# Kernel optimization log

Hardware: AMD Instinct MI355X
Metric: run time of the kernel (lower is better)

Reference implementation:

```python
import jax, jax.numpy as jnp
import numpy as np
from jax import lax

H = 100          # hidden_size
IN = 100         # input_size
NUM_LAYERS = 2   # options.LSTMLayer
B = 128
T = 1024


def _uniform(key, shape, bound):
    return jax.random.uniform(key, shape, jnp.float32, -bound, bound)


def setup_inputs() -> dict:
    key = jax.random.key(0)
    ks = jax.random.split(key, 16)
    bound = 1.0 / np.sqrt(H)  # torch nn.LSTM default init
    x = jax.random.normal(ks[0], (B, IN, T), jnp.float32)
    # layer 0: input dim IN; layer 1: input dim 2*H. Stacked over 2 directions.
    w_ih0 = _uniform(ks[1], (2, 4 * H, IN), bound)
    w_hh0 = _uniform(ks[2], (2, 4 * H, H), bound)
    b0 = _uniform(ks[3], (2, 4 * H), bound) + _uniform(ks[4], (2, 4 * H), bound)  # b_ih + b_hh
    w_ih1 = _uniform(ks[5], (2, 4 * H, 2 * H), bound)
    w_hh1 = _uniform(ks[6], (2, 4 * H, H), bound)
    b1 = _uniform(ks[7], (2, 4 * H), bound) + _uniform(ks[8], (2, 4 * H), bound)
    return {"x": x, "w_ih0": w_ih0, "w_hh0": w_hh0, "b0": b0,
            "w_ih1": w_ih1, "w_hh1": w_hh1, "b1": b1}


def _lstm_dir(x, w_ih, w_hh, b):
    # x: (T,B,D). Precompute input-to-gate GEMM once, then scan the recurrence.
    gx = jnp.einsum('tbd,gd->tbg', x, w_ih) + b  # (T,B,4H)
    h0 = jnp.zeros((x.shape[1], H), x.dtype)
    c0 = jnp.zeros((x.shape[1], H), x.dtype)

    def step(carry, g):
        h, c = carry
        gates = g + h @ w_hh.T
        i, f, gg, o = jnp.split(gates, 4, axis=-1)  # torch gate order i,f,g,o
        i = jax.nn.sigmoid(i)
        f = jax.nn.sigmoid(f)
        gg = jnp.tanh(gg)
        o = jax.nn.sigmoid(o)
        c = f * c + i * gg
        h = o * jnp.tanh(c)
        return (h, c), h

    _, hs = lax.scan(step, (h0, c0), gx)
    return hs  # (T,B,H)


def _bilstm_layer(x, w_ih, w_hh, b):
    fwd = _lstm_dir(x, w_ih[0], w_hh[0], b[0])
    bwd = _lstm_dir(x[::-1], w_ih[1], w_hh[1], b[1])[::-1]
    return jnp.concatenate([fwd, bwd], axis=-1)  # (T,B,2H)


def reference(x, w_ih0, w_hh0, b0, w_ih1, w_hh1, b1):
    # x: (B, 100, T) -> permute([2,0,1]) -> (T, B, 100)
    h = jnp.transpose(x, (2, 0, 1))
    h = _bilstm_layer(h, w_ih0, w_hh0, b0)
    h = _bilstm_layer(h, w_ih1, w_hh1, b1)
    return h  # (T, B, 2H), matching nn.LSTM `output`
```

## Files before the change

kernel.cpp:

```cpp
#include <hip/hip_runtime.h>
#include <hip/hip_bf16.h>
#include <stdint.h>

typedef unsigned short ushort_t;
typedef __attribute__((ext_vector_type(8))) short short8;
typedef __attribute__((ext_vector_type(4))) short short4_t;
typedef __attribute__((ext_vector_type(4))) float f32x4;

#define TT 1024
#define BB 128
#define NG 400
#define HID 100

#define ALIGN256(x) ((((size_t)(x)) + 255) & ~(size_t)255)

static const size_t WS_FLAG = 0;
static const size_t WS_XT   = 4096;
static const size_t WS_OUT0 = WS_XT   + (size_t)1024 * 128 * 128 * 2;
static const size_t WS_GX   = WS_OUT0 + (size_t)1024 * 128 * 256 * 2;
static const size_t WS_WIH0 = WS_GX   + (size_t)2 * 1024 * 128 * 400 * 2;
static const size_t WS_WHH  = WS_WIH0 + (size_t)2 * 400 * 128 * 2;
static const size_t WS_WIH1 = WS_WHH  + (size_t)2 * 2 * 400 * 128 * 2;
static const size_t WS_BIAS = WS_WIH1 + (size_t)2 * 400 * 256 * 2;

__device__ __forceinline__ float bf2f(ushort_t v) {
  return __builtin_bit_cast(float, ((unsigned)v) << 16);
}
__device__ __forceinline__ ushort_t f2bf(float f) {
  unsigned u = __builtin_bit_cast(unsigned, f);
  u += 0x7FFF + ((u >> 16) & 1);
  return (ushort_t)(u >> 16);
}
__device__ __forceinline__ ushort_t ldbf(const void* p, size_t i, int isbf) {
  return isbf ? ((const ushort_t*)p)[i] : f2bf(((const float*)p)[i]);
}
__device__ __forceinline__ float ldf(const void* p, size_t i, int isbf) {
  return isbf ? bf2f(((const ushort_t*)p)[i]) : ((const float*)p)[i];
}
__device__ __forceinline__ float fexp2(float x) {
#if __has_builtin(__builtin_amdgcn_exp2f)
  return __builtin_amdgcn_exp2f(x);
#else
  return __exp2f(x);
#endif
}
__device__ __forceinline__ float frcp(float x) {
#if __has_builtin(__builtin_amdgcn_rcpf)
  return __builtin_amdgcn_rcpf(x);
#else
  return 1.0f / x;
#endif
}
__device__ __forceinline__ float sigm(float x) {
  return frcp(1.0f + fexp2(-1.44269504f * x));
}
__device__ __forceinline__ float tanh_(float x) {
  return 1.0f - 2.0f * frcp(1.0f + fexp2(2.88539008f * x));
}

__global__ __launch_bounds__(256) void detect_dtype(const ushort_t* __restrict__ x,
                                                    int* __restrict__ flag) {
  __shared__ int cnt;
  if (threadIdx.x == 0) cnt = 0;
  __syncthreads();
  int local = 0;
  for (int i = threadIdx.x; i < 4096; i += 256) {
    ushort_t u = x[2 * i];
    int e = (u >> 7) & 0xFF;
    if (e >= 0x66 && e <= 0x85) local++;
  }
  atomicAdd(&cnt, local);
  __syncthreads();
  if (threadIdx.x == 0) *flag = (cnt >= 2048) ? 1 : 0;
}

__global__ __launch_bounds__(256) void prep_weights(
    const void* __restrict__ wih0, const void* __restrict__ whh0,
    const void* __restrict__ b0,   const void* __restrict__ wih1,
    const void* __restrict__ whh1, const void* __restrict__ b1,
    ushort_t* __restrict__ WIH0, ushort_t* __restrict__ WHH,
    ushort_t* __restrict__ WIH1, float* __restrict__ BIAS,
    const int* __restrict__ flag)
{
  const int isbf = *flag;
  int tid = blockIdx.x * blockDim.x + threadIdx.x;
  int nth = gridDim.x * blockDim.x;
  for (int idx = tid; idx < 2 * NG * 128; idx += nth) {
    int k = idx & 127; int np = (idx >> 7) % NG; int d = idx / (NG * 128);
    int n = (np & 3) * HID + (np >> 2);
    WIH0[idx] = (k < HID) ? ldbf(wih0, (size_t)(d * NG + n) * 100 + k, isbf) : (ushort_t)0;
  }
  for (int idx = tid; idx < 2 * 2 * NG * 128; idx += nth) {
    int k = idx & 127; int np = (idx >> 7) % NG; int dl = idx / (NG * 128);
    int d = dl & 1; int l = dl >> 1;
    int n = (np & 3) * HID + (np >> 2);
    const void* src = l ? whh1 : whh0;
    WHH[idx] = (k < HID) ? ldbf(src, (size_t)(d * NG + n) * 100 + k, isbf) : (ushort_t)0;
  }
  for (int idx = tid; idx < 2 * NG * 256; idx += nth) {
    int k = idx & 255; int np = (idx >> 8) % NG; int d = idx / (NG * 256);
    int n = (np & 3) * HID + (np >> 2);
    int c = (k < 100) ? k : ((k >= 128 && k < 228) ? (k - 28) : -1);
    WIH1[idx] = (c >= 0) ? ldbf(wih1, (size_t)(d * NG + n) * 200 + c, isbf) : (ushort_t)0;
  }
  for (int idx = tid; idx < 2 * 2 * NG; idx += nth) {
    int np = idx % NG; int dl = idx / NG; int d = dl & 1; int l = dl >> 1;
    int n = (np & 3) * HID + (np >> 2);
    BIAS[idx] = ldf(l ? b1 : b0, d * NG + n, isbf);
  }
}

__global__ __launch_bounds__(256) void pack_x(const void* __restrict__ x,
                                              ushort_t* __restrict__ xT,
                                              const int* __restrict__ flag)
{
  __shared__ ushort_t tile[100][68];
  const int isbf = *flag;
  const int b = blockIdx.x;
  const int t0 = blockIdx.y << 6;
  for (int i = threadIdx.x; i < 100 * 64; i += 256) {
    int k = i >> 6, t = i & 63;
    tile[k][t] = ldbf(x, ((size_t)b * 100 + k) * TT + t0 + t, isbf);
  }
  __syncthreads();
  for (int i = threadIdx.x; i < 128 * 64; i += 256) {
    int k = i & 127, t = i >> 7;
    xT[((size_t)(t0 + t) * BB + b) * 128 + k] = (k < 100) ? tile[k][t] : (ushort_t)0;
  }
}

__global__ __launch_bounds__(256) void gemm_gx(
    const ushort_t* __restrict__ A, const ushort_t* __restrict__ W,
    const float* __restrict__ BIASL, ushort_t* __restrict__ gxo, int kpad)
{
  const int mtile = blockIdx.x;
  const int d = blockIdx.y;
  const int w = threadIdx.x >> 6;
  const int lane = threadIdx.x & 63;
  const int quad = lane >> 4;
  const int lm = lane & 15;
  const int m0 = mtile * 16;
  const int nkt = kpad >> 5;

  f32x4 acc[7];
#pragma unroll
  for (int i = 0; i < 7; i++) acc[i] = (f32x4){0.f, 0.f, 0.f, 0.f};

  const ushort_t* Wd = W + (size_t)d * NG * kpad;
  const ushort_t* Ap = A + (size_t)(m0 + lm) * kpad + quad * 8;

  for (int kt = 0; kt < nkt; kt++) {
    short8 a = *(const short8*)(Ap + kt * 32);
#pragma unroll
    for (int i = 0; i < 7; i++) {
      int nt = w + 4 * i; if (nt >= 25) nt = 0;
      short8 bb = *(const short8*)(Wd + (size_t)(nt * 16 + lm) * kpad + kt * 32 + quad * 8);
      acc[i] = __builtin_amdgcn_mfma_f32_16x16x32_bf16(a, bb, acc[i], 0, 0, 0);
    }
  }

  const int t = mtile >> 3, bg = mtile & 7;
  ushort_t* go = gxo + (((size_t)d * TT + t) * 8 + bg) * 6400;
  const float* bd = BIASL + d * NG;
  const int qr = lm >> 2, gam = lm & 3;
#pragma unroll
  for (int i = 0; i < 7; i++) {
    int nt = w + 4 * i;
    if (nt >= 25) break;
    int n = nt * 16 + lm;
    float bias = bd[n];
#pragma unroll
    for (int r = 0; r < 4; r++)
      go[(nt * 64 + (quad * 4 + r) * 4 + qr) * 4 + gam] = f2bf(acc[i][r] + bias);
  }
}

template<bool F32OUT>
__global__ __launch_bounds__(512, 1) void lstm_layer(
    const ushort_t* __restrict__ gx, const ushort_t* __restrict__ WHHl,
    void* __restrict__ outp, int ostride, int colmult)
{
  const int dir = blockIdx.x >> 3;
  const int bg = blockIdx.x & 7;
  const int b0 = bg << 4;
  const int w = threadIdx.x >> 6;
  const int lane = threadIdx.x & 63;
  const int quad = lane >> 4;
  const int lm = lane & 15;
  const int ocol = dir * colmult;

  __shared__ ushort_t hbuf[2][16][136];
  for (int i = threadIdx.x; i < 2 * 16 * 136; i += 512) ((ushort_t*)hbuf)[i] = 0;

  short8 afragW[4][4];
  int nts[4];
#pragma unroll
  for (int i = 0; i < 4; i++) {
    int nt = (i < 3) ? (w + 8 * i) : 24;
    nts[i] = nt;
    const ushort_t* wp = WHHl + ((size_t)dir * NG + nt * 16 + lm) * 128;
#pragma unroll
    for (int kt = 0; kt < 4; kt++)
      afragW[i][kt] = *(const short8*)(wp + kt * 32 + quad * 8);
  }

  int loff[4];
#pragma unroll
  for (int i = 0; i < 4; i++) loff[i] = (nts[i] * 64 + lm * 4 + quad) * 4;

  float cst[4] = {0.f, 0.f, 0.f, 0.f};
  const ushort_t* gxd = gx + ((size_t)dir * TT * 8 + bg) * 6400;

  short4_t pf[4];
  {
    int tt0 = dir ? (TT - 1) : 0;
    const ushort_t* gp = gxd + (size_t)tt0 * 8 * 6400;
#pragma unroll
    for (int i = 0; i < 4; i++) pf[i] = *(const short4_t*)(gp + loff[i]);
  }

  __syncthreads();

  for (int t = 0; t < TT; t++) {
    const int tt = dir ? (TT - 1 - t) : t;
    const int pb = t & 1;

    f32x4 acc[4];
#pragma unroll
    for (int i = 0; i < 4; i++) {
#pragma unroll
      for (int r = 0; r < 4; r++) acc[i][r] = bf2f((ushort_t)pf[i][r]);
    }

    if (t + 1 < TT) {
      int tn = dir ? (TT - 2 - t) : (t + 1);
      const ushort_t* gp = gxd + (size_t)tn * 8 * 6400;
#pragma unroll
      for (int i = 0; i < 4; i++) pf[i] = *(const short4_t*)(gp + loff[i]);
    }

    short8 bfr[4];
#pragma unroll
    for (int kt = 0; kt < 4; kt++)
      bfr[kt] = *(const short8*)(&hbuf[pb][lm][kt * 32 + quad * 8]);

#pragma unroll
    for (int i = 0; i < 4; i++) {
      if (i == 3 && w != 0) continue;
#pragma unroll
      for (int kt = 0; kt < 4; kt++)
        acc[i] = __builtin_amdgcn_mfma_f32_16x16x32_bf16(afragW[i][kt], bfr[kt], acc[i], 0, 0, 0);
    }

#pragma unroll
    for (int i = 0; i < 4; i++) {
      if (i == 3 && w != 0) continue;
      float gi = acc[i][0], gf = acc[i][1], gg = acc[i][2], go = acc[i][3];
      float cn = sigm(gf) * cst[i] + sigm(gi) * tanh_(gg);
      cst[i] = cn;
      float h = sigm(go) * tanh_(cn);
      int j = nts[i] * 4 + quad;
      hbuf[pb ^ 1][lm][j] = f2bf(h);
      size_t oidx = ((size_t)tt * BB + b0 + lm) * ostride + ocol + j;
      if (F32OUT) ((float*)outp)[oidx] = h;
      else        ((ushort_t*)outp)[oidx] = f2bf(h);
    }
    __syncthreads();
  }
}

extern "C" void kernel_launch(void* const* d_in, const int* in_sizes, int n_in,
                              void* d_out, int out_size, void* d_ws, size_t ws_size,
                              hipStream_t stream) {
  const void* x_raw    = d_in[0];
  const void* wih0_raw = d_in[1];
  const void* whh0_raw = d_in[2];
  const void* b0_raw   = d_in[3];
  const void* wih1_raw = d_in[4];
  const void* whh1_raw = d_in[5];
  const void* b1_raw   = d_in[6];

  char* ws = (char*)d_ws;
  int*      FLAG = (int*)(ws + WS_FLAG);
  ushort_t* xT   = (ushort_t*)(ws + WS_XT);
  ushort_t* out0 = (ushort_t*)(ws + WS_OUT0);
  ushort_t* gx   = (ushort_t*)(ws + WS_GX);
  ushort_t* WIH0 = (ushort_t*)(ws + WS_WIH0);
  ushort_t* WHH  = (ushort_t*)(ws + WS_WHH);
  ushort_t* WIH1 = (ushort_t*)(ws + WS_WIH1);
  float*    BIAS = (float*)(ws + WS_BIAS);

  detect_dtype<<<1, 256, 0, stream>>>((const ushort_t*)x_raw, FLAG);

  prep_weights<<<256, 256, 0, stream>>>(wih0_raw, whh0_raw, b0_raw,
                                        wih1_raw, whh1_raw, b1_raw,
                                        WIH0, WHH, WIH1, BIAS, FLAG);
  pack_x<<<dim3(128, 16), 256, 0, stream>>>(x_raw, xT, FLAG);

  gemm_gx<<<dim3(8192, 2), 256, 0, stream>>>(xT, WIH0, BIAS, gx, 128);
  lstm_layer<false><<<16, 512, 0, stream>>>(gx, WHH, out0, 256, 128);
  gemm_gx<<<dim3(8192, 2), 256, 0, stream>>>(out0, WIH1, BIAS + 2 * NG, gx, 256);
  lstm_layer<true><<<16, 512, 0, stream>>>(gx, WHH + (size_t)2 * NG * 128, d_out, 200, 100);
}
```

Measured before the change: 3.036 ms.

## Merge both LSTM directions into one 1024-thread workgroup per batch group

The recurrent LSTM kernel now runs both directions in a single 1024-thread workgroup: warps 0-7 handle the forward direction and 8-15 the backward, each with its own double-buffered h tile in LDS. Eight workgroups are launched instead of sixteen. A separate kernel zeroes the padding columns of the intermediate layer-0 output buffer, likely so they are no longer rewritten elsewhere. The change shifts how the recurrence maps onto CUs. It also makes every workgroup-wide barrier wait for both directions, and the heavier 16-warp blocks may change register pressure and latency.

```diff
diff --git a/kernel.cpp b/kernel.cpp
--- a/kernel.cpp
+++ b/kernel.cpp
@@ -1,6 +1,7 @@
 #include <hip/hip_runtime.h>
 #include <hip/hip_bf16.h>
 #include <stdint.h>
+#include <stddef.h>
 
 typedef unsigned short ushort_t;
 typedef __attribute__((ext_vector_type(8))) short short8;
@@ -129,6 +130,15 @@
   }
 }
 
+__global__ __launch_bounds__(256) void zero_out0_pads(unsigned* __restrict__ o) {
+  int tid = blockIdx.x * blockDim.x + threadIdx.x;
+  int r = tid >> 5, u = tid & 31;
+  if (u < 28) {
+    int cu = (u < 14) ? (50 + u) : (100 + u);
+    o[(size_t)r * 128 + cu] = 0u;
+  }
+}
+
 __global__ __launch_bounds__(256) void gemm_gx(
     const ushort_t* __restrict__ A, const ushort_t* __restrict__ W,
     const float* __restrict__ BIASL, ushort_t* __restrict__ gxo, int kpad)
@@ -176,21 +186,23 @@
 }
 
 template<bool F32OUT>
-__global__ __launch_bounds__(512, 1) void lstm_layer(
+__global__ __launch_bounds__(1024, 1) void lstm_layer(
     const ushort_t* __restrict__ gx, const ushort_t* __restrict__ WHHl,
     void* __restrict__ outp, int ostride, int colmult)
 {
-  const int dir = blockIdx.x >> 3;
-  const int bg = blockIdx.x & 7;
+  const int bg = blockIdx.x;
   const int b0 = bg << 4;
-  const int w = threadIdx.x >> 6;
+  const int wid = threadIdx.x >> 6;
+  const int dir = wid >> 3;
+  const int w = wid & 7;
   const int lane = threadIdx.x & 63;
   const int quad = lane >> 4;
   const int lm = lane & 15;
   const int ocol = dir * colmult;
-
-  __shared__ ushort_t hbuf[2][16][136];
-  for (int i = threadIdx.x; i < 2 * 16 * 136; i += 512) ((ushort_t*)hbuf)[i] = 0;
+  const int xw = dir ? 2 : 0;
+
+  __shared__ ushort_t hbuf[2][2][16][136];
+  for (int i = threadIdx.x; i < 2 * 2 * 16 * 136; i += 1024) ((ushort_t*)hbuf)[i] = 0;
 
   short8 afragW[4][4];
   int nts[4];
@@ -242,11 +254,11 @@
     short8 bfr[4];
 #pragma unroll
     for (int kt = 0; kt < 4; kt++)
-      bfr[kt] = *(const short8*)(&hbuf[pb][lm][kt * 32 + quad * 8]);
+      bfr[kt] = *(const short8*)(&hbuf[dir][pb][lm][kt * 32 + quad * 8]);
 
 #pragma unroll
     for (int i = 0; i < 4; i++) {
-      if (i == 3 && w != 0) continue;
+      if (i == 3 && w != xw) continue;
 #pragma unroll
       for (int kt = 0; kt < 4; kt++)
         acc[i] = __builtin_amdgcn_mfma_f32_16x16x32_bf16(afragW[i][kt], bfr[kt], acc[i], 0, 0, 0);
@@ -254,13 +266,13 @@
 
 #pragma unroll
     for (int i = 0; i < 4; i++) {
-      if (i == 3 && w != 0) continue;
+      if (i == 3 && w != xw) continue;
       float gi = acc[i][0], gf = acc[i][1], gg = acc[i][2], go = acc[i][3];
       float cn = sigm(gf) * cst[i] + sigm(gi) * tanh_(gg);
       cst[i] = cn;
       float h = sigm(go) * tanh_(cn);
       int j = nts[i] * 4 + quad;
-      hbuf[pb ^ 1][lm][j] = f2bf(h);
+      hbuf[dir][pb ^ 1][lm][j] = f2bf(h);
       size_t oidx = ((size_t)tt * BB + b0 + lm) * ostride + ocol + j;
       if (F32OUT) ((float*)outp)[oidx] = h;
       else        ((ushort_t*)outp)[oidx] = f2bf(h);
@@ -296,9 +308,10 @@
                                         wih1_raw, whh1_raw, b1_raw,
                                         WIH0, WHH, WIH1, BIAS, FLAG);
   pack_x<<<dim3(128, 16), 256, 0, stream>>>(x_raw, xT, FLAG);
+  zero_out0_pads<<<16384, 256, 0, stream>>>((unsigned*)out0);
 
   gemm_gx<<<dim3(8192, 2), 256, 0, stream>>>(xT, WIH0, BIAS, gx, 128);
-  lstm_layer<false><<<16, 512, 0, stream>>>(gx, WHH, out0, 256, 128);
+  lstm_layer<false><<<8, 1024, 0, stream>>>(gx, WHH, out0, 256, 128);
   gemm_gx<<<dim3(8192, 2), 256, 0, stream>>>(out0, WIH1, BIAS + 2 * NG, gx, 256);
-  lstm_layer<true><<<16, 512, 0, stream>>>(gx, WHH + (size_t)2 * NG * 128, d_out, 200, 100);
-}
+  lstm_layer<true><<<8, 1024, 0, stream>>>(gx, WHH + (size_t)2 * NG * 128, d_out, 200, 100);
+}
```

After: 5.553 ms. +82.9%, slower.
